# Optimization experiments

Hardware: AMD Instinct MI355X
Metric: run time of the kernel (lower is better)

The kernel has to match this reference:

```python
import jax, jax.numpy as jnp
import numpy as np
from itertools import product

N_CODONS = 2
ORDER = 2
N_STATES = 25          # calc_number_of_states() with nCodons=2
ALPHA6 = 6             # alphabet_size + 2
OFFSET = 8 + 3 * N_CODONS       # 14, first insert state
TERM1 = OFFSET + 3 * (N_CODONS + 1)  # 23, terminal_1 state

CODE = {'A': [0], 'C': [1], 'G': [2], 'T': [3], 'N': [0, 1, 2, 3], 'X': [5]}


def _state_entries(state, emissions, x_must_preceed):
    ems = ['N'] * (ORDER - len(emissions) + 1) + list(emissions)[-(ORDER + 1):]
    allowed = [[state]]
    for i, e in enumerate(ems):
        allowed.append(CODE[e] + ([4] if i < ORDER - x_must_preceed else []))
    out = []
    for x in product(*allowed):
        found, ok = False, True
        for i in range(1, ORDER + 1):
            if found and x[i] == 4:
                ok = False
                break
            if x[i] != 4:
                found = True
        if ok:
            out.append(x)
    return out


def _emission_index_spec():
    entries, k = [], 0
    def add(state, ems, xp, trainable=True):
        nonlocal k
        ids = _state_entries(state, ems, xp)
        for t, x in enumerate(ids):
            entries.append((x, k + t if trainable else -1))
        if trainable:
            k += len(ids)
    add(0, 'N', 0); add(1, 'A', 0); add(2, 'AT', 0); add(3, 'ATG', 0, False)
    add(4, 'ATGN', 0); add(5, 'ATGNN', 0)
    for s in range(6, 6 + N_CODONS * 3 - 2):
        add(s, 'N', 0)
    add(4 + 3 * N_CODONS, 'T', ORDER)
    add(5 + 3 * N_CODONS, 'TA', ORDER); add(5 + 3 * N_CODONS, 'TG', ORDER)
    add(6 + 3 * N_CODONS, 'TAA', ORDER, False)
    add(6 + 3 * N_CODONS, 'TAG', ORDER, False)
    add(6 + 3 * N_CODONS, 'TGA', ORDER, False)
    add(7 + 3 * N_CODONS, 'N', ORDER)
    for s in range(8 + 3 * N_CODONS, 8 + 3 * N_CODONS + 3 * (N_CODONS + 1)):
        add(s, 'N', 0)
    for i in range(1, ORDER + 1):
        add(TERM1, 'X' * i, ORDER)
    add(TERM1 + 1, 'X' * (ORDER + 1), ORDER, False)
    idx = np.array([e[0] for e in entries], dtype=np.int32)
    widx = np.array([e[1] for e in entries], dtype=np.int32)
    return idx, widx

EM_IDX, EM_WIDX = _emission_index_spec()


def build_A(w):
    # sparse transition structure -> row-softmax over nonzeros -> dense [25,25]
    idx, vals = [], []
    def add(i, j, v):
        idx.append((i, j)); vals.append(v)
    n, k = N_CODONS, 0
    add(0, 0, 1 - w[k]); add(0, 1, w[k]); k += 1
    add(1, 2, 1.0); add(2, 3, 1.0)
    for i in range(n):
        add(3 + 3 * i, 4 + 3 * i, w[k + i])
    k += n
    for i in range(n):
        add(4 + 3 * i, 5 + 3 * i, 1.0)
    for i in range(n):
        add(5 + 3 * i, 6 + 3 * i, 1.0)
    for i in range(n + 1):
        add(3 + 3 * i, OFFSET + 3 * i, w[k + i])
    k += n + 1
    add(3 + 3 * n, 4 + 3 * n, 1 - w[k - 1])
    for i in range(n + 1):
        add(OFFSET + 3 * i, OFFSET + 1 + 3 * i, 1.0)
    for i in range(n + 1):
        add(OFFSET + 1 + 3 * i, OFFSET + 2 + 3 * i, 1.0)
    for i in range(n + 1):
        add(OFFSET + 2 + 3 * i, 4 + 3 * i, w[k + i])
    for i in range(n + 1):
        add(OFFSET + 2 + 3 * i, OFFSET + 3 * i, 1 - w[k + i])
    k += n + 1
    i_del = [3 + 3 * i for i in range(n) for _ in range(n - i)]
    j_del = [4 + 3 * j for i in range(1, n + 1) for j in range(i, n + 1)]
    for i, j in zip(i_del, j_del):
        add(i, j, 1 - w[k] * w[k] ** ((j - i) // 3))
    k += 1
    add(4 + 3 * n, 5 + 3 * n, 1.0); add(5 + 3 * n, 6 + 3 * n, 1.0)
    add(6 + 3 * n, 7 + 3 * n, 1.0)
    add(7 + 3 * n, 7 + 3 * n, 1.0); add(7 + 3 * n, TERM1, 1.0)
    add(TERM1, TERM1, 1.0); add(TERM1, TERM1 + 1, 1.0)
    add(TERM1 + 1, TERM1 + 1, 1.0)
    rows = np.array([i for i, _ in idx]); cols = np.array([j for _, j in idx])
    logits = jnp.stack([jnp.asarray(v, jnp.float32) for v in vals])
    M = jnp.full((N_STATES, N_STATES), -jnp.inf, jnp.float32).at[rows, cols].set(logits)
    A = jax.nn.softmax(M, axis=-1)
    return jnp.where(jnp.isfinite(M), A, 0.0)


def build_B(w):
    # sparse emission values (trainable weights or fixed 1), per-state softmax over nonzeros
    vals = jnp.where(EM_WIDX >= 0, w[np.clip(EM_WIDX, 0, None)], 1.0)
    rows = EM_IDX[:, 0]
    flat = EM_IDX[:, 1] * 36 + EM_IDX[:, 2] * 6 + EM_IDX[:, 3]
    M = jnp.full((N_STATES, ALPHA6 ** 3), -jnp.inf, jnp.float32).at[rows, flat].set(vals)
    B = jax.nn.softmax(M, axis=-1)
    return jnp.where(jnp.isfinite(M), B, 0.0)  # [25, 216]


def build_I(w):
    n_init = 3 + 3 * N_CODONS  # states 0..8 get initial mass
    p = jax.nn.softmax(w[:n_init])
    return jnp.zeros((N_STATES,), jnp.float32).at[:n_init].set(p)


def _forward(transition_kernel, emission_kernel, init_kernel, tokens):
    A = build_A(transition_kernel)
    Bf = build_B(emission_kernel)
    I = build_I(init_kernel)
    Bt, T = tokens.shape
    pad = jnp.full((Bt, ORDER), 4, tokens.dtype)  # '4' = no preceding emission
    tp = jnp.concatenate([pad, tokens], axis=1)
    flat = tp[:, :-2] * 36 + tp[:, 1:-1] * 6 + tp[:, 2:]  # [Bt, T]
    E = jnp.moveaxis(Bf.T[flat], 1, 0)  # [T, Bt, 25]
    alpha = I[None, :] * E[0]
    s = alpha.sum(-1, keepdims=True)
    alpha = alpha / s
    ll = jnp.log(s[..., 0])
    def step(carry, e):
        a, ll = carry
        a = (a @ A) * e
        s = a.sum(-1, keepdims=True)
        return (a / s, ll + jnp.log(s[..., 0])), None
    (alpha, ll), _ = jax.lax.scan(step, (alpha, ll), E[1:])
    return ll  # [Bt] per-sequence log-likelihood


def setup_inputs() -> dict:
    key = jax.random.key(0)
    k1, k2, k3, k4 = jax.random.split(key, 4)
    return {
        'transition_kernel': jax.random.normal(k1, (10,), jnp.float32) * 0.05,
        'emission_kernel': jax.random.normal(k2, (5400,), jnp.float32) * 0.05,
        'init_kernel': jax.random.normal(k3, (25,), jnp.float32) * 0.05,
        'tokens': jax.random.randint(k4, (512, 2048), 0, 4, jnp.int32),
    }


def reference(transition_kernel, emission_kernel, init_kernel, tokens):
    return _forward(transition_kernel, emission_kernel, init_kernel, tokens)
```

## Files before the change

### kernel.cpp

```cpp
#include <hip/hip_runtime.h>
#include <hip/hip_bf16.h>
#include <math.h>


#define NSTATES 25
#define NLIVE   23
#define NFLAT   216
#define NPACK   100
#define TLEN    2048
#define NSEQ    512
#define CHUNKS  16
#define CLEN    128

struct WMap { short m[NSTATES * NFLAT]; };

constexpr WMap make_wmap() {
  WMap w{};
  for (int i = 0; i < NSTATES * NFLAT; i++) w.m[i] = -2;
  const unsigned char ST[29] = {0,1,2,3,4,5,6,7,8,9,10,11,11,12,12,12,13,
                                14,15,16,17,18,19,20,21,22,23,23,24};
  const unsigned char M1[29] = {0x1F,0x1F,0x1F,0x11,0x18,0x14,0x1F,0x1F,0x1F,
                                0x1F,0x0F,0x0F,0x0F,0x08,0x08,0x08,0x0F,
                                0x1F,0x1F,0x1F,0x1F,0x1F,0x1F,0x1F,0x1F,0x1F,
                                0x0F,0x0F,0x20};
  const unsigned char M2[29] = {0x1F,0x1F,0x11,0x18,0x14,0x1F,0x1F,0x1F,0x1F,
                                0x1F,0x0F,0x08,0x08,0x01,0x01,0x04,0x0F,
                                0x1F,0x1F,0x1F,0x1F,0x1F,0x1F,0x1F,0x1F,0x1F,
                                0x0F,0x20,0x20};
  const unsigned char M3[29] = {0x0F,0x01,0x08,0x04,0x0F,0x0F,0x0F,0x0F,0x0F,
                                0x0F,0x08,0x01,0x04,0x01,0x04,0x01,0x0F,
                                0x0F,0x0F,0x0F,0x0F,0x0F,0x0F,0x0F,0x0F,0x0F,
                                0x20,0x20,0x20};
  const unsigned char TR[29] = {1,1,1,0,1,1,1,1,1,1,1,1,1,0,0,0,1,
                                1,1,1,1,1,1,1,1,1,1,1,0};
  int k = 0;
  for (int s = 0; s < 29; s++) {
    for (int c1 = 0; c1 < 6; c1++) {
      if (!((M1[s] >> c1) & 1)) continue;
      for (int c2 = 0; c2 < 6; c2++) {
        if (!((M2[s] >> c2) & 1)) continue;
        if (c1 != 4 && c2 == 4) continue;
        for (int c3 = 0; c3 < 6; c3++) {
          if (!((M3[s] >> c3) & 1)) continue;
          w.m[ST[s] * NFLAT + c1 * 36 + c2 * 6 + c3] =
              TR[s] ? (short)(k++) : (short)-1;
        }
      }
    }
  }
  return w;
}
__device__ __constant__ WMap WMAP = make_wmap();

__device__ __forceinline__ unsigned short f2bf(float x) {
  unsigned int u = __float_as_uint(x);
  u += 0x7fffu + ((u >> 16) & 1u);
  return (unsigned short)(u >> 16);
}

__device__ __forceinline__ void hmm_step(float (&a)[NLIVE], const float (&w)[21],
                                         const float* __restrict__ bt, int idx) {
  const float* er = bt + (idx << 5);
  float4 e0 = *(const float4*)(er + 0);
  float4 e1 = *(const float4*)(er + 4);
  float4 e2 = *(const float4*)(er + 8);
  float4 e3 = *(const float4*)(er + 12);
  float4 e4 = *(const float4*)(er + 16);
  float4 e5 = *(const float4*)(er + 20);

  float n0  = a[0]*w[0];
  float n1  = a[0]*w[1];
  float n4  = a[3]*w[2]  + a[16]*w[13];
  float n7  = a[3]*w[4]  + a[6]*w[6]  + a[19]*w[15];
  float n10 = a[3]*w[5]  + a[6]*w[8]  + a[9]*w[10] + a[22]*w[17];
  float n13 = a[12]      + a[13]*w[11];
  float n14 = a[3]*w[3]  + a[16]*w[14];
  float n17 = a[6]*w[7]  + a[19]*w[16];
  float n20 = a[9]*w[9]  + a[22]*w[18];
  float o2 = a[1],  o3 = a[2],  o5 = a[4],  o6 = a[5];
  float o8 = a[7],  o9 = a[8],  o11 = a[10], o12 = a[11];
  float o15 = a[14], o16 = a[15], o18 = a[17], o19 = a[18];
  float o21 = a[20], o22 = a[21];

  a[0] = n0 * e0.x;  a[1] = n1 * e0.y;  a[2] = o2 * e0.z;  a[3] = o3 * e0.w;
  a[4] = n4 * e1.x;  a[5] = o5 * e1.y;  a[6] = o6 * e1.z;  a[7] = n7 * e1.w;
  a[8] = o8 * e2.x;  a[9] = o9 * e2.y;  a[10] = n10 * e2.z; a[11] = o11 * e2.w;
  a[12] = o12 * e3.x; a[13] = n13 * e3.y; a[14] = n14 * e3.z; a[15] = o15 * e3.w;
  a[16] = o16 * e4.x; a[17] = n17 * e4.y; a[18] = o18 * e4.z; a[19] = o19 * e4.w;
  a[20] = n20 * e5.x; a[21] = o21 * e5.y; a[22] = o22 * e5.z;
}

__device__ __forceinline__ void renorm(float (&a)[NLIVE], float& L) {
  float s = (((a[0]+a[1])+(a[2]+a[3])) + ((a[4]+a[5])+(a[6]+a[7])))
          + (((a[8]+a[9])+(a[10]+a[11])) + ((a[12]+a[13])+(a[14]+a[15])))
          + (((a[16]+a[17])+(a[18]+a[19])) + ((a[20]+a[21])+a[22]));
  if (s > 0.0f) {
    L += __logf(s);
    float r = __fdividef(1.0f, s);
    #pragma unroll
    for (int j = 0; j < NLIVE; j++) a[j] *= r;
  } else {
    L = -3.0e38f;
  }
}

#define STEP(nt_) { int nt = (nt_); hmm_step(a, w, sBt, (c12 << 2) + nt); \
                    c12 = p2 * 5 + nt; p2 = nt; }

__global__ __launch_bounds__(512)
void hmm_kernel(const float* __restrict__ wT, const float* __restrict__ wE,
                const float* __restrict__ wI, const int* __restrict__ tokens,
                float* __restrict__ out) {
  __shared__ __align__(16) float          sBt[NPACK * 32];
  __shared__ __align__(16) unsigned short sT[CHUNKS * NLIVE * 24];
  __shared__ float sL[CHUNKS * NLIVE];
  __shared__ float sAW[24];
  __shared__ float sI[32];

  const int tid   = threadIdx.x;
  const int seq   = blockIdx.x;
  const int chunk = tid >> 5;
  const int row   = tid & 31;
  const int* trow = tokens + (size_t)seq * TLEN;

  for (int st = chunk; st < NSTATES; st += 16) {
    float part = 0.0f;
    for (int c = row; c < NFLAT; c += 32) {
      short m = WMAP.m[st * NFLAT + c];
      if (m == -1) part += expf(1.0f);
      else if (m >= 0) part += expf(wE[m]);
    }
    #pragma unroll
    for (int m = 1; m < 32; m <<= 1) part += __shfl_xor(part, m, 32);
    float inv = 1.0f / part;
    for (int i = row; i < NPACK; i += 32) {
      int c12 = i >> 2, nt = i & 3;
      int p1 = c12 / 5, p2v = c12 - 5 * p1;
      int flat = p1 * 36 + p2v * 6 + nt;
      short m = WMAP.m[st * NFLAT + flat];
      float v = 0.0f;
      if (m == -1) v = expf(1.0f);
      else if (m >= 0) v = expf(wE[m]);
      sBt[i * 32 + st] = v * inv;
    }
  }
  if (tid == 480) {
    const float w0 = wT[0], w1 = wT[1], w2 = wT[2], w3 = wT[3], w4 = wT[4];
    const float w5 = wT[5], w6 = wT[6], w7 = wT[7], w8 = wT[8], w9 = wT[9];
    { float e0 = expf(1.0f - w0), e1 = expf(w0), is = 1.0f / (e0 + e1);
      sAW[0] = e0 * is; sAW[1] = e1 * is; }
    { float e4 = expf(w1), e14 = expf(w3);
      float e7 = expf(1.0f - w9 * w9), e10 = expf(1.0f - w9 * w9 * w9);
      float is = 1.0f / (e4 + e14 + e7 + e10);
      sAW[2] = e4 * is;  sAW[3] = e14 * is;
      sAW[4] = e7 * is;  sAW[5] = e10 * is; }
    { float e7 = expf(w2), e17 = expf(w4), e10 = expf(1.0f - w9 * w9);
      float is = 1.0f / (e7 + e17 + e10);
      sAW[6] = e7 * is; sAW[7] = e17 * is; sAW[8] = e10 * is; }
    { float e20 = expf(w5), e10 = expf(1.0f - w5), is = 1.0f / (e20 + e10);
      sAW[9] = e20 * is; sAW[10] = e10 * is; }
    sAW[11] = 0.5f; sAW[12] = 0.5f;
    { float e4 = expf(w6), e14 = expf(1.0f - w6), is = 1.0f / (e4 + e14);
      sAW[13] = e4 * is; sAW[14] = e14 * is; }
    { float e7 = expf(w7), e17 = expf(1.0f - w7), is = 1.0f / (e7 + e17);
      sAW[15] = e7 * is; sAW[16] = e17 * is; }
    { float e10 = expf(w8), e20 = expf(1.0f - w8), is = 1.0f / (e10 + e20);
      sAW[17] = e10 * is; sAW[18] = e20 * is; }
    sAW[19] = 0.5f; sAW[20] = 0.5f;
  } else if (tid == 481) {
    float e[9], s = 0.0f;
    for (int i = 0; i < 9; i++) { e[i] = expf(wI[i]); s += e[i]; }
    float inv = 1.0f / s;
    for (int i = 0; i < 9; i++) sI[i] = e[i] * inv;
    for (int i = 9; i < 32; i++) sI[i] = 0.0f;
  }
  __syncthreads();

  float w[21];
  #pragma unroll
  for (int i = 0; i < 21; i++)
    w[i] = __uint_as_float(
        (unsigned)__builtin_amdgcn_readfirstlane(__float_as_uint(sAW[i])));

  const int t0 = chunk * CLEN;

  float a[NLIVE];
  #pragma unroll
  for (int j = 0; j < NLIVE; j++) a[j] = 0.0f;
  if (row < NLIVE) a[row] = 1.0f;
  float L = 0.0f;

  int c12, p2;
  int4 q0 = *(const int4*)(trow + t0);
  int4 q1 = *(const int4*)(trow + t0 + 4);

  int b = 0;
  if (chunk == 0) {
    c12 = 20 + q0.x; p2 = q0.x;
    STEP(q0.y); STEP(q0.z); STEP(q0.w);
    STEP(q1.x); STEP(q1.y); STEP(q1.z); STEP(q1.w);
    renorm(a, L);
    b = 1;
    q0 = *(const int4*)(trow + 8);
    q1 = *(const int4*)(trow + 12);
  } else {
    int2 pp = *(const int2*)(trow + t0 - 2);
    c12 = pp.x * 5 + pp.y; p2 = pp.y;
  }

  for (; b < CLEN / 8; b++) {
    int4 n0 = q0, n1 = q1;
    if (b + 1 < CLEN / 8) {
      n0 = *(const int4*)(trow + t0 + (b + 1) * 8);
      n1 = *(const int4*)(trow + t0 + (b + 1) * 8 + 4);
    }
    STEP(q0.x); STEP(q0.y); STEP(q0.z); STEP(q0.w);
    STEP(q1.x); STEP(q1.y); STEP(q1.z); STEP(q1.w);
    renorm(a, L);
    q0 = n0; q1 = n1;
  }

  if (row < NLIVE) {
    const int base = (chunk * NLIVE + row) * 24;
    #pragma unroll
    for (int k = 0; k < 11; k++) {
      ushort2 p; p.x = f2bf(a[2 * k]); p.y = f2bf(a[2 * k + 1]);
      *(ushort2*)&sT[base + 2 * k] = p;
    }
    { ushort2 p; p.x = f2bf(a[22]); p.y = 0; *(ushort2*)&sT[base + 22] = p; }
    sL[chunk * NLIVE + row] = L;
  }
  __syncthreads();

  if (tid < 64) {
    const int lane = tid;
    const bool act = (lane < NLIVE);
    const int jc   = act ? lane : 0;

    const int tok0 = trow[0];
    const int idx0 = 96 + tok0;

    float v = act ? sI[lane] * sBt[idx0 * 32 + lane] : 0.0f;
    float s = v;
    #pragma unroll
    for (int m = 1; m < 32; m <<= 1) s += __shfl_xor(s, m, 32);
    float ll = __logf(s);
    v = act ? v * __fdividef(1.0f, s) : 0.0f;

    for (int c = 0; c < CHUNKS; c++) {
      float Lj  = act ? sL[c * NLIVE + lane] : -3.0e38f;
      float key = (act && v > 0.0f) ? Lj : -3.0e38f;
      float mx = key;
      #pragma unroll
      for (int m = 1; m < 32; m <<= 1) mx = fmaxf(mx, __shfl_xor(mx, m, 32));
      float wgt = (act && v > 0.0f) ? v * __expf(Lj - mx) : 0.0f;

      float nv = 0.0f;
      #pragma unroll
      for (int r = 0; r < NLIVE; r++) {
        float wr = __shfl(wgt, r, 64);
        nv += wr * __uint_as_float(((unsigned)sT[(c * NLIVE + r) * 24 + jc]) << 16);
      }
      float nva = act ? nv : 0.0f;
      float s2 = nva;
      #pragma unroll
      for (int m = 1; m < 32; m <<= 1) s2 += __shfl_xor(s2, m, 32);
      ll += mx + __logf(s2);
      v = act ? nv * __fdividef(1.0f, s2) : 0.0f;
    }

    if (lane == 0) out[seq] = ll;
  }
}

extern "C" void kernel_launch(void* const* d_in, const int* in_sizes, int n_in,
                              void* d_out, int out_size, void* d_ws, size_t ws_size,
                              hipStream_t stream) {
  const float* wT = (const float*)d_in[0];
  const float* wE = (const float*)d_in[1];
  const float* wI = (const float*)d_in[2];
  const int* tokens = (const int*)d_in[3];
  float* out = (float*)d_out;
  (void)d_ws; (void)ws_size;

  hmm_kernel<<<NSEQ, 512, 0, stream>>>(wT, wE, wI, tokens, out);
}
```

Baseline: 138.2 us.

## Prefetch emission rows one step ahead, scale emissions by 16, renorm every 16 steps

```diff
diff --git a/kernel.cpp b/kernel.cpp
--- a/kernel.cpp
+++ b/kernel.cpp
@@ -11,6 +11,8 @@
 #define NSEQ    512
 #define CHUNKS  16
 #define CLEN    128
+
+#define LOG16 2.772588722239781f
 
 struct WMap { short m[NSTATES * NFLAT]; };
 
@@ -58,16 +60,15 @@
   return (unsigned short)(u >> 16);
 }
 
-__device__ __forceinline__ void hmm_step(float (&a)[NLIVE], const float (&w)[21],
-                                         const float* __restrict__ bt, int idx) {
-  const float* er = bt + (idx << 5);
-  float4 e0 = *(const float4*)(er + 0);
-  float4 e1 = *(const float4*)(er + 4);
-  float4 e2 = *(const float4*)(er + 8);
-  float4 e3 = *(const float4*)(er + 12);
-  float4 e4 = *(const float4*)(er + 16);
-  float4 e5 = *(const float4*)(er + 20);
-
+__device__ __forceinline__ void ldrow(float4 (&R)[6],
+                                      const float* __restrict__ bt, int idx) {
+  const float4* er = (const float4*)(bt + (idx << 5));
+  R[0] = er[0]; R[1] = er[1]; R[2] = er[2];
+  R[3] = er[3]; R[4] = er[4]; R[5] = er[5];
+}
+
+__device__ __forceinline__ void hmm_step_r(float (&a)[NLIVE], const float (&w)[21],
+                                           const float4 (&R)[6]) {
   float n0  = a[0]*w[0];
   float n1  = a[0]*w[1];
   float n4  = a[3]*w[2]  + a[16]*w[13];
@@ -82,12 +83,18 @@
   float o15 = a[14], o16 = a[15], o18 = a[17], o19 = a[18];
   float o21 = a[20], o22 = a[21];
 
-  a[0] = n0 * e0.x;  a[1] = n1 * e0.y;  a[2] = o2 * e0.z;  a[3] = o3 * e0.w;
-  a[4] = n4 * e1.x;  a[5] = o5 * e1.y;  a[6] = o6 * e1.z;  a[7] = n7 * e1.w;
-  a[8] = o8 * e2.x;  a[9] = o9 * e2.y;  a[10] = n10 * e2.z; a[11] = o11 * e2.w;
-  a[12] = o12 * e3.x; a[13] = n13 * e3.y; a[14] = n14 * e3.z; a[15] = o15 * e3.w;
-  a[16] = o16 * e4.x; a[17] = n17 * e4.y; a[18] = o18 * e4.z; a[19] = o19 * e4.w;
-  a[20] = n20 * e5.x; a[21] = o21 * e5.y; a[22] = o22 * e5.z;
+  a[0]  = n0  * R[0].x;  a[1]  = n1  * R[0].y;
+  a[2]  = o2  * R[0].z;  a[3]  = o3  * R[0].w;
+  a[4]  = n4  * R[1].x;  a[5]  = o5  * R[1].y;
+  a[6]  = o6  * R[1].z;  a[7]  = n7  * R[1].w;
+  a[8]  = o8  * R[2].x;  a[9]  = o9  * R[2].y;
+  a[10] = n10 * R[2].z;  a[11] = o11 * R[2].w;
+  a[12] = o12 * R[3].x;  a[13] = n13 * R[3].y;
+  a[14] = n14 * R[3].z;  a[15] = o15 * R[3].w;
+  a[16] = o16 * R[4].x;  a[17] = n17 * R[4].y;
+  a[18] = o18 * R[4].z;  a[19] = o19 * R[4].w;
+  a[20] = n20 * R[5].x;  a[21] = o21 * R[5].y;
+  a[22] = o22 * R[5].z;
 }
 
 __device__ __forceinline__ void renorm(float (&a)[NLIVE], float& L) {
@@ -104,10 +111,12 @@
   }
 }
 
-#define STEP(nt_) { int nt = (nt_); hmm_step(a, w, sBt, (c12 << 2) + nt); \
-                    c12 = p2 * 5 + nt; p2 = nt; }
-
-__global__ __launch_bounds__(512)
+#define LDONLY(Rn, nt_) { int nt = (nt_); ldrow(Rn, sBt, (c12 << 2) + nt); \
+                          c12 = p2 * 5 + nt; p2 = nt; }
+#define LDSTEP(Rn, Rc, nt_) { int nt = (nt_); ldrow(Rn, sBt, (c12 << 2) + nt); \
+                              c12 = p2 * 5 + nt; p2 = nt; hmm_step_r(a, w, Rc); }
+
+__global__ __launch_bounds__(512, 4)
 void hmm_kernel(const float* __restrict__ wT, const float* __restrict__ wE,
                 const float* __restrict__ wI, const int* __restrict__ tokens,
                 float* __restrict__ out) {
@@ -132,7 +141,7 @@
     }
     #pragma unroll
     for (int m = 1; m < 32; m <<= 1) part += __shfl_xor(part, m, 32);
-    float inv = 1.0f / part;
+    float inv = 16.0f / part;
     for (int i = row; i < NPACK; i += 32) {
       int c12 = i >> 2, nt = i & 3;
       int p1 = c12 / 5, p2v = c12 - 5 * p1;
@@ -190,6 +199,7 @@
   if (row < NLIVE) a[row] = 1.0f;
   float L = 0.0f;
 
+  float4 A[6], B[6];
   int c12, p2;
   int4 q0 = *(const int4*)(trow + t0);
   int4 q1 = *(const int4*)(trow + t0 + 4);
@@ -197,9 +207,14 @@
   int b = 0;
   if (chunk == 0) {
     c12 = 20 + q0.x; p2 = q0.x;
-    STEP(q0.y); STEP(q0.z); STEP(q0.w);
-    STEP(q1.x); STEP(q1.y); STEP(q1.z); STEP(q1.w);
-    renorm(a, L);
+    LDONLY(A, q0.y);
+    LDSTEP(B, A, q0.z);
+    LDSTEP(A, B, q0.w);
+    LDSTEP(B, A, q1.x);
+    LDSTEP(A, B, q1.y);
+    LDSTEP(B, A, q1.z);
+    LDSTEP(A, B, q1.w);
+    hmm_step_r(a, w, A);
     b = 1;
     q0 = *(const int4*)(trow + 8);
     q1 = *(const int4*)(trow + 12);
@@ -214,11 +229,20 @@
       n0 = *(const int4*)(trow + t0 + (b + 1) * 8);
       n1 = *(const int4*)(trow + t0 + (b + 1) * 8 + 4);
     }
-    STEP(q0.x); STEP(q0.y); STEP(q0.z); STEP(q0.w);
-    STEP(q1.x); STEP(q1.y); STEP(q1.z); STEP(q1.w);
-    renorm(a, L);
+    LDONLY(A, q0.x);
+    LDSTEP(B, A, q0.y);
+    LDSTEP(A, B, q0.z);
+    LDSTEP(B, A, q0.w);
+    LDSTEP(A, B, q1.x);
+    LDSTEP(B, A, q1.y);
+    LDSTEP(A, B, q1.z);
+    LDSTEP(B, A, q1.w);
+    hmm_step_r(a, w, B);
+    if (b & 1) renorm(a, L);
     q0 = n0; q1 = n1;
   }
+
+  if (L > -1.0e38f) L -= (chunk == 0 ? 127.0f : 128.0f) * LOG16;
 
   if (row < NLIVE) {
     const int base = (chunk * NLIVE + row) * 24;
@@ -244,7 +268,7 @@
     float s = v;
     #pragma unroll
     for (int m = 1; m < 32; m <<= 1) s += __shfl_xor(s, m, 32);
-    float ll = __logf(s);
+    float ll = __logf(s) - LOG16;
     v = act ? v * __fdividef(1.0f, s) : 0.0f;
 
     for (int c = 0; c < CHUNKS; c++) {
```

Result: faster. 134.9 us (-2.4%).

## Pack HMM state into float2 vectors, prescale emissions, and halve renormalization

Applied to the files above, without the earlier changes.

```diff
diff --git a/kernel.cpp b/kernel.cpp
--- a/kernel.cpp
+++ b/kernel.cpp
@@ -2,6 +2,9 @@
 #include <hip/hip_bf16.h>
 #include <math.h>
 
+
+typedef float v2f __attribute__((ext_vector_type(2)));
+typedef float v4f __attribute__((ext_vector_type(4)));
 
 #define NSTATES 25
 #define NLIVE   23
@@ -11,6 +14,11 @@
 #define NSEQ    512
 #define CHUNKS  16
 #define CLEN    128
+
+#define LOG16 2.772588722239781f
+
+__device__ __constant__ int PERMC[24] = {1,4,2,5,3,6,7,10,8,11,9,12,
+                                         14,17,15,18,16,19,20,0,21,13,22,23};
 
 struct WMap { short m[NSTATES * NFLAT]; };
 
@@ -52,62 +60,72 @@
 }
 __device__ __constant__ WMap WMAP = make_wmap();
 
+__device__ __constant__ int POSA[NLIVE] = {19,0,2,4,1,3,5,6,8,10,7,9,11,21,
+                                           12,14,16,13,15,17,18,20,22};
+
 __device__ __forceinline__ unsigned short f2bf(float x) {
   unsigned int u = __float_as_uint(x);
   u += 0x7fffu + ((u >> 16) & 1u);
   return (unsigned short)(u >> 16);
 }
 
-__device__ __forceinline__ void hmm_step(float (&a)[NLIVE], const float (&w)[21],
-                                         const float* __restrict__ bt, int idx) {
-  const float* er = bt + (idx << 5);
-  float4 e0 = *(const float4*)(er + 0);
-  float4 e1 = *(const float4*)(er + 4);
-  float4 e2 = *(const float4*)(er + 8);
-  float4 e3 = *(const float4*)(er + 12);
-  float4 e4 = *(const float4*)(er + 16);
-  float4 e5 = *(const float4*)(er + 20);
-
-  float n0  = a[0]*w[0];
-  float n1  = a[0]*w[1];
-  float n4  = a[3]*w[2]  + a[16]*w[13];
-  float n7  = a[3]*w[4]  + a[6]*w[6]  + a[19]*w[15];
-  float n10 = a[3]*w[5]  + a[6]*w[8]  + a[9]*w[10] + a[22]*w[17];
-  float n13 = a[12]      + a[13]*w[11];
-  float n14 = a[3]*w[3]  + a[16]*w[14];
-  float n17 = a[6]*w[7]  + a[19]*w[16];
-  float n20 = a[9]*w[9]  + a[22]*w[18];
-  float o2 = a[1],  o3 = a[2],  o5 = a[4],  o6 = a[5];
-  float o8 = a[7],  o9 = a[8],  o11 = a[10], o12 = a[11];
-  float o15 = a[14], o16 = a[15], o18 = a[17], o19 = a[18];
-  float o21 = a[20], o22 = a[21];
-
-  a[0] = n0 * e0.x;  a[1] = n1 * e0.y;  a[2] = o2 * e0.z;  a[3] = o3 * e0.w;
-  a[4] = n4 * e1.x;  a[5] = o5 * e1.y;  a[6] = o6 * e1.z;  a[7] = n7 * e1.w;
-  a[8] = o8 * e2.x;  a[9] = o9 * e2.y;  a[10] = n10 * e2.z; a[11] = o11 * e2.w;
-  a[12] = o12 * e3.x; a[13] = n13 * e3.y; a[14] = n14 * e3.z; a[15] = o15 * e3.w;
-  a[16] = o16 * e4.x; a[17] = n17 * e4.y; a[18] = o18 * e4.z; a[19] = o19 * e4.w;
-  a[20] = n20 * e5.x; a[21] = o21 * e5.y; a[22] = o22 * e5.z;
-}
-
-__device__ __forceinline__ void renorm(float (&a)[NLIVE], float& L) {
-  float s = (((a[0]+a[1])+(a[2]+a[3])) + ((a[4]+a[5])+(a[6]+a[7])))
-          + (((a[8]+a[9])+(a[10]+a[11])) + ((a[12]+a[13])+(a[14]+a[15])))
-          + (((a[16]+a[17])+(a[18]+a[19])) + ((a[20]+a[21])+a[22]));
+struct Wp {
+  v2f w01, wA, wB, wC, wD, wE, wF;
+  float w4, w5, w8, w11;
+};
+
+__device__ __forceinline__ void step_pk(v2f (&Q)[12], const v4f (&F)[6],
+                                        const Wp& W) {
+  float a0 = Q[9].y,  a3 = Q[2].x,  a6 = Q[2].y,  a9 = Q[5].x;
+  float a12 = Q[5].y, a13 = Q[10].y, a16 = Q[8].x, a19 = Q[8].y, a22 = Q[11].x;
+  float q9x = Q[9].x, q10x = Q[10].x;
+
+  v2f t01 = a0 * W.w01;
+  v2f t44 = a3 * W.wA + a16 * W.wB;
+  v2f t77 = a6 * W.wC + a19 * W.wD;
+  float n7  = fmaf(a3, W.w4, t77.x);
+  v2f tAA = a9 * W.wE + a22 * W.wF;
+  float n10 = fmaf(a3, W.w5, fmaf(a6, W.w8, tAA.x));
+  float n13 = fmaf(a13, W.w11, a12);
+
+  v2f nQ1 = Q[0] * __builtin_shufflevector(F[0], F[0], 2, 3);
+  v2f nQ2 = Q[1] * __builtin_shufflevector(F[1], F[1], 0, 1);
+  v2f nQ4 = Q[3] * __builtin_shufflevector(F[2], F[2], 0, 1);
+  v2f nQ5 = Q[4] * __builtin_shufflevector(F[2], F[2], 2, 3);
+  v2f nQ7 = Q[6] * __builtin_shufflevector(F[3], F[3], 2, 3);
+  v2f nQ8 = Q[7] * __builtin_shufflevector(F[4], F[4], 0, 1);
+
+  Q[0]  = (v2f){ t01.y * F[0].x, t44.x * F[0].y };
+  Q[3]  = (v2f){ n7    * F[1].z, n10   * F[1].w };
+  Q[6]  = (v2f){ t44.y * F[3].x, t77.y * F[3].y };
+  Q[9]  = (v2f){ tAA.y * F[4].z, t01.x * F[4].w };
+  Q[10] = (v2f){ q9x   * F[5].x, n13   * F[5].y };
+  Q[11].x = q10x * F[5].z;
+  Q[1] = nQ1; Q[2] = nQ2; Q[4] = nQ4; Q[5] = nQ5; Q[7] = nQ7; Q[8] = nQ8;
+}
+
+__device__ __forceinline__ void renorm_pk(v2f (&Q)[12], float& L) {
+  v2f acc = ((Q[0] + Q[1]) + (Q[2] + Q[3])) + ((Q[4] + Q[5]) + (Q[6] + Q[7]))
+          + ((Q[8] + Q[9]) + (Q[10] + Q[11]));
+  float s = acc.x + acc.y;
   if (s > 0.0f) {
     L += __logf(s);
     float r = __fdividef(1.0f, s);
     #pragma unroll
-    for (int j = 0; j < NLIVE; j++) a[j] *= r;
+    for (int k = 0; k < 12; k++) Q[k] *= r;
   } else {
     L = -3.0e38f;
   }
 }
 
-#define STEP(nt_) { int nt = (nt_); hmm_step(a, w, sBt, (c12 << 2) + nt); \
-                    c12 = p2 * 5 + nt; p2 = nt; }
-
-__global__ __launch_bounds__(512)
+#define LDROW(F, nt_) { int nt = (nt_); \
+  const v4f* er = (const v4f*)(sBt + (((c12 << 2) + nt) << 5)); \
+  F[0] = er[0]; F[1] = er[1]; F[2] = er[2]; \
+  F[3] = er[3]; F[4] = er[4]; F[5] = er[5]; \
+  c12 = p2 * 5 + nt; p2 = nt; }
+#define LDSTEP(Fn, Fc, nt_) { LDROW(Fn, nt_); step_pk(Q, Fc, W); }
+
+__global__ __launch_bounds__(512, 4)
 void hmm_kernel(const float* __restrict__ wT, const float* __restrict__ wE,
                 const float* __restrict__ wI, const int* __restrict__ tokens,
                 float* __restrict__ out) {
@@ -123,7 +141,8 @@
   const int row   = tid & 31;
   const int* trow = tokens + (size_t)seq * TLEN;
 
-  for (int st = chunk; st < NSTATES; st += 16) {
+  for (int st = chunk; st < NLIVE; st += 16) {
+    const int pos = POSA[st];
     float part = 0.0f;
     for (int c = row; c < NFLAT; c += 32) {
       short m = WMAP.m[st * NFLAT + c];
@@ -132,7 +151,7 @@
     }
     #pragma unroll
     for (int m = 1; m < 32; m <<= 1) part += __shfl_xor(part, m, 32);
-    float inv = 1.0f / part;
+    float inv = 16.0f / part;
     for (int i = row; i < NPACK; i += 32) {
       int c12 = i >> 2, nt = i & 3;
       int p1 = c12 / 5, p2v = c12 - 5 * p1;
@@ -141,9 +160,10 @@
       float v = 0.0f;
       if (m == -1) v = expf(1.0f);
       else if (m >= 0) v = expf(wE[m]);
-      sBt[i * 32 + st] = v * inv;
-    }
-  }
+      sBt[i * 32 + pos] = v * inv;
+    }
+  }
+  for (int i = tid; i < NPACK; i += 512) sBt[i * 32 + 23] = 0.0f;
   if (tid == 480) {
     const float w0 = wT[0], w1 = wT[1], w2 = wT[2], w3 = wT[3], w4 = wT[4];
     const float w5 = wT[5], w6 = wT[6], w7 = wT[7], w8 = wT[8], w9 = wT[9];
@@ -181,15 +201,27 @@
   for (int i = 0; i < 21; i++)
     w[i] = __uint_as_float(
         (unsigned)__builtin_amdgcn_readfirstlane(__float_as_uint(sAW[i])));
+  Wp W;
+  W.w01 = (v2f){w[0],  w[1]};
+  W.wA  = (v2f){w[2],  w[3]};
+  W.wB  = (v2f){w[13], w[14]};
+  W.wC  = (v2f){w[6],  w[7]};
+  W.wD  = (v2f){w[15], w[16]};
+  W.wE  = (v2f){w[10], w[9]};
+  W.wF  = (v2f){w[17], w[18]};
+  W.w4 = w[4]; W.w5 = w[5]; W.w8 = w[8]; W.w11 = w[11];
 
   const int t0 = chunk * CLEN;
 
-  float a[NLIVE];
+  v2f Q[12];
   #pragma unroll
-  for (int j = 0; j < NLIVE; j++) a[j] = 0.0f;
-  if (row < NLIVE) a[row] = 1.0f;
+  for (int k = 0; k < 12; k++) {
+    Q[k].x = (row == PERMC[2 * k]) ? 1.0f : 0.0f;
+    Q[k].y = (row == PERMC[2 * k + 1]) ? 1.0f : 0.0f;
+  }
   float L = 0.0f;
 
+  v4f FA[6], FB[6];
   int c12, p2;
   int4 q0 = *(const int4*)(trow + t0);
   int4 q1 = *(const int4*)(trow + t0 + 4);
@@ -197,9 +229,14 @@
   int b = 0;
   if (chunk == 0) {
     c12 = 20 + q0.x; p2 = q0.x;
-    STEP(q0.y); STEP(q0.z); STEP(q0.w);
-    STEP(q1.x); STEP(q1.y); STEP(q1.z); STEP(q1.w);
-    renorm(a, L);
+    LDROW(FA, q0.y);
+    LDSTEP(FB, FA, q0.z);
+    LDSTEP(FA, FB, q0.w);
+    LDSTEP(FB, FA, q1.x);
+    LDSTEP(FA, FB, q1.y);
+    LDSTEP(FB, FA, q1.z);
+    LDSTEP(FA, FB, q1.w);
+    step_pk(Q, FA, W);
     b = 1;
     q0 = *(const int4*)(trow + 8);
     q1 = *(const int4*)(trow + 12);
@@ -214,20 +251,28 @@
       n0 = *(const int4*)(trow + t0 + (b + 1) * 8);
       n1 = *(const int4*)(trow + t0 + (b + 1) * 8 + 4);
     }
-    STEP(q0.x); STEP(q0.y); STEP(q0.z); STEP(q0.w);
-    STEP(q1.x); STEP(q1.y); STEP(q1.z); STEP(q1.w);
-    renorm(a, L);
+    LDROW(FA, q0.x);
+    LDSTEP(FB, FA, q0.y);
+    LDSTEP(FA, FB, q0.z);
+    LDSTEP(FB, FA, q0.w);
+    LDSTEP(FA, FB, q1.x);
+    LDSTEP(FB, FA, q1.y);
+    LDSTEP(FA, FB, q1.z);
+    LDSTEP(FB, FA, q1.w);
+    step_pk(Q, FB, W);
+    if (b & 1) renorm_pk(Q, L);
     q0 = n0; q1 = n1;
   }
+
+  if (L > -1.0e38f) L -= (chunk == 0 ? 127.0f : 128.0f) * LOG16;
 
   if (row < NLIVE) {
     const int base = (chunk * NLIVE + row) * 24;
     #pragma unroll
-    for (int k = 0; k < 11; k++) {
-      ushort2 p; p.x = f2bf(a[2 * k]); p.y = f2bf(a[2 * k + 1]);
+    for (int k = 0; k < 12; k++) {
+      ushort2 p; p.x = f2bf(Q[k].x); p.y = f2bf(Q[k].y);
       *(ushort2*)&sT[base + 2 * k] = p;
     }
-    { ushort2 p; p.x = f2bf(a[22]); p.y = 0; *(ushort2*)&sT[base + 22] = p; }
     sL[chunk * NLIVE + row] = L;
   }
   __syncthreads();
@@ -235,16 +280,20 @@
   if (tid < 64) {
     const int lane = tid;
     const bool act = (lane < NLIVE);
-    const int jc   = act ? lane : 0;
+
+    int jp = 23;
+    #pragma unroll
+    for (int pos = 0; pos < 23; pos++)
+      if (PERMC[pos] == lane) jp = pos;
 
     const int tok0 = trow[0];
     const int idx0 = 96 + tok0;
 
-    float v = act ? sI[lane] * sBt[idx0 * 32 + lane] : 0.0f;
+    float v = act ? sI[lane] * sBt[idx0 * 32 + jp] : 0.0f;
     float s = v;
     #pragma unroll
     for (int m = 1; m < 32; m <<= 1) s += __shfl_xor(s, m, 32);
-    float ll = __logf(s);
+    float ll = __logf(s) - LOG16;
     v = act ? v * __fdividef(1.0f, s) : 0.0f;
 
     for (int c = 0; c < CHUNKS; c++) {
@@ -259,7 +308,7 @@
       #pragma unroll
       for (int r = 0; r < NLIVE; r++) {
         float wr = __shfl(wgt, r, 64);
-        nv += wr * __uint_as_float(((unsigned)sT[(c * NLIVE + r) * 24 + jc]) << 16);
+        nv += wr * __uint_as_float(((unsigned)sT[(c * NLIVE + r) * 24 + jp]) << 16);
       }
       float nva = act ? nv : 0.0f;
       float s2 = nva;
```

Measured after the change: 121.6 us. 12.1% less time.
